# Kernel tuning notes

Measured on AMD Instinct MI355X. Metric: run time of the kernel, lower is better.

Reference implementation:

```python
import jax, jax.numpy as jnp
import numpy as np

STRIDES = (4, 8, 16, 32)
OUT = 7
RATIO = 2  # sampling_ratio per bin dim (ROIAlignV2)
P = OUT * RATIO  # sample points per spatial dim


def _bilinear_axis(coord, size):
    # ROIAlign semantics: zero contribution outside [-1, size], clamp into [0, size-1]
    valid = ((coord > -1.0) & (coord < size)).astype(coord.dtype)
    c = jnp.clip(coord, 0.0, size - 1)
    i0 = jnp.floor(c).astype(jnp.int32)
    i1 = jnp.minimum(i0 + 1, size - 1)
    frac = c - i0.astype(coord.dtype)
    return i0, i1, (1.0 - frac) * valid, frac * valid


def _roi_align(fmap, bidx, boxes, stride):
    """ROIAlignV2 (aligned=True, sampling_ratio=2). fmap: [B,H,W,C], boxes: [N,4] in image coords."""
    H, W = fmap.shape[1], fmap.shape[2]
    x1 = boxes[:, 0] / stride - 0.5
    y1 = boxes[:, 1] / stride - 0.5
    x2 = boxes[:, 2] / stride - 0.5
    y2 = boxes[:, 3] / stride - 0.5
    steps = (jnp.arange(P, dtype=fmap.dtype) + 0.5) / P  # [P] uniform sample centers
    px = x1[:, None] + (x2 - x1)[:, None] * steps  # [N,P]
    py = y1[:, None] + (y2 - y1)[:, None] * steps  # [N,P]
    ix0, ix1, wx0, wx1 = _bilinear_axis(px, W)
    iy0, iy1, wy0, wy1 = _bilinear_axis(py, H)
    b = bidx[:, None, None]

    def g(yi, xi):
        return fmap[b, yi[:, :, None], xi[:, None, :]]  # [N,P,P,C]

    val = ((wy0[:, :, None] * wx0[:, None, :])[..., None] * g(iy0, ix0)
           + (wy0[:, :, None] * wx1[:, None, :])[..., None] * g(iy0, ix1)
           + (wy1[:, :, None] * wx0[:, None, :])[..., None] * g(iy1, ix0)
           + (wy1[:, :, None] * wx1[:, None, :])[..., None] * g(iy1, ix1))
    N, C = boxes.shape[0], fmap.shape[3]
    pooled = val.reshape(N, OUT, RATIO, OUT, RATIO, C).mean(axis=(2, 4))  # avg within each bin
    return pooled.transpose(0, 3, 1, 2).reshape(N, C * OUT * OUT)  # torch [N,C,7,7].flatten(1)


def _head(fms, rois, fc1_w, fc1_b, fc2_w, fc2_b, p_w, p_b):
    bidx = rois[:, 0].astype(jnp.int32)
    boxes = rois[:, 1:5]
    w = boxes[:, 2] - boxes[:, 0]
    h = boxes[:, 3] - boxes[:, 1]
    # standard FPN level assignment: k = floor(4 + log2(sqrt(area)/224)), clamp [2,5]
    k = jnp.floor(4.0 + jnp.log2(jnp.sqrt(jnp.maximum(w * h, 1e-6)) / 224.0))
    lvl = jnp.clip(k, 2.0, 5.0).astype(jnp.int32) - 2  # 0->stride4 ... 3->stride32
    pooled = jnp.stack([_roi_align(fm.transpose(0, 2, 3, 1), bidx, boxes, s)
                        for fm, s in zip(fms, STRIDES)])  # [4,N,D]
    pool5 = pooled[lvl, jnp.arange(rois.shape[0])]  # [N,D] select per-roi level
    fc1 = jax.nn.relu(pool5 @ fc1_w.T + fc1_b)
    fc2 = jax.nn.relu(fc1 @ fc2_w.T + fc2_b)
    return fc2 @ p_w.T + p_b  # prob: [N, 5*n*nheads]


def setup_inputs():
    key = jax.random.key(0)
    ks = jax.random.split(key, 12)
    B, C = 2, 256
    ImH, ImW = 768, 1280
    N = 1024
    NUM_CLASSES, NHEADS = 2, 2
    D = C * OUT * OUT
    fms = [jax.random.normal(ks[i], (B, C, ImH // s, ImW // s), dtype=jnp.float32)
           for i, s in enumerate(STRIDES)]
    # boxes with log-uniform sizes in [32, 512] px, clipped to image
    wh = jnp.exp(jax.random.uniform(ks[4], (N, 2), minval=float(np.log(32.0)), maxval=float(np.log(512.0))))
    cxy = jax.random.uniform(ks[5], (N, 2)) * jnp.array([ImW, ImH], jnp.float32)
    x1 = jnp.clip(cxy[:, 0] - wh[:, 0] / 2, 0.0, ImW - 2.0)
    y1 = jnp.clip(cxy[:, 1] - wh[:, 1] / 2, 0.0, ImH - 2.0)
    x2 = jnp.clip(cxy[:, 0] + wh[:, 0] / 2, x1 + 1.0, ImW - 1.0)
    y2 = jnp.clip(cxy[:, 1] + wh[:, 1] / 2, y1 + 1.0, ImH - 1.0)
    bidx = jax.random.randint(ks[6], (N,), 0, B).astype(jnp.float32)
    rois = jnp.stack([bidx, x1, y1, x2, y2], axis=1)
    fc1_w = jax.random.normal(ks[7], (1024, D), dtype=jnp.float32) / np.sqrt(D).astype(np.float32)
    fc1_b = jnp.zeros((1024,), jnp.float32)
    fc2_w = jax.random.normal(ks[8], (1024, 1024), dtype=jnp.float32) / 32.0
    fc2_b = jnp.zeros((1024,), jnp.float32)
    p_w = jax.random.normal(ks[9], (5 * NUM_CLASSES * NHEADS, 1024), dtype=jnp.float32) / 32.0
    p_b = jnp.zeros((5 * NUM_CLASSES * NHEADS,), jnp.float32)
    return {"fm0": fms[0], "fm1": fms[1], "fm2": fms[2], "fm3": fms[3], "rois": rois,
            "fc1_w": fc1_w, "fc1_b": fc1_b, "fc2_w": fc2_w, "fc2_b": fc2_b,
            "p_w": p_w, "p_b": p_b}


def reference(fm0, fm1, fm2, fm3, rois, fc1_w, fc1_b, fc2_w, fc2_b, p_w, p_b):
    return _head((fm0, fm1, fm2, fm3), rois, fc1_w, fc1_b, fc2_w, fc2_b, p_w, p_b)
```

## Files before the change

### kernel.cpp

```cpp
#include <hip/hip_runtime.h>
#include <hip/hip_bf16.h>
#include <cstddef>
#include <cstdint>


#define NROIS 1024
#define C_CH  256
#define OUTP  7
#define DFEAT (C_CH * OUTP * OUTP)
#define HID   1024
#define NCLS  20

__device__ __forceinline__ unsigned short f2bf(float x) {
    union { float f; uint32_t u; } v; v.f = x;
    uint32_t r = v.u + 0x7fffu + ((v.u >> 16) & 1u);
    return (unsigned short)(r >> 16);
}
__device__ __forceinline__ float bf2f(unsigned short h) {
    union { uint32_t u; float f; } v; v.u = ((uint32_t)h) << 16;
    return v.f;
}

__device__ __forceinline__ void g2lds16(const void* g, void* l) {
    __builtin_amdgcn_global_load_lds(
        (const __attribute__((address_space(1))) void*)g,
        (__attribute__((address_space(3))) void*)l,
        16, 0, 0);
}

typedef __attribute__((ext_vector_type(8))) short bf16x8;
typedef __attribute__((ext_vector_type(4))) float f32x4;

__global__ __launch_bounds__(256) void roi_pool_split(
    const float* __restrict__ fm0, const float* __restrict__ fm1,
    const float* __restrict__ fm2, const float* __restrict__ fm3,
    const float* __restrict__ rois,
    unsigned short* __restrict__ ph, unsigned short* __restrict__ pl)
{
    const int roi = blockIdx.x;
    const int cq  = blockIdx.y;
    const int t   = threadIdx.x;

    __shared__ float s_box[5];
    __shared__ int   s_ix0[16], s_ix1[16], s_iy0[16], s_iy1[16];
    __shared__ float s_wx0[16], s_wx1[16], s_wy0[16], s_wy1[16];

    if (t < 5) s_box[t] = rois[(size_t)roi * 5 + t];
    __syncthreads();

    const int   b   = (int)s_box[0];
    const float bx1 = s_box[1], by1 = s_box[2], bx2 = s_box[3], by2 = s_box[4];

    const float w = bx2 - bx1, h = by2 - by1;
    float kf = floorf(4.0f + log2f(sqrtf(fmaxf(w * h, 1e-6f)) / 224.0f));
    kf = fminf(fmaxf(kf, 2.0f), 5.0f);
    const int lvl    = (int)kf - 2;
    const int stride = 4 << lvl;
    const int H  = 768  / stride;
    const int Wd = 1280 / stride;
    const float* fm = (lvl == 0) ? fm0 : (lvl == 1) ? fm1 : (lvl == 2) ? fm2 : fm3;

    if (t < 14) {
        const float x1s = bx1 / (float)stride - 0.5f;
        const float x2s = bx2 / (float)stride - 0.5f;
        const float coord = x1s + (x2s - x1s) * (((float)t + 0.5f) / 14.0f);
        const float valid = (coord > -1.0f && coord < (float)Wd) ? 1.0f : 0.0f;
        const float cc = fminf(fmaxf(coord, 0.0f), (float)(Wd - 1));
        const int i0 = (int)floorf(cc);
        s_ix0[t] = i0; s_ix1[t] = min(i0 + 1, Wd - 1);
        const float fr = cc - (float)i0;
        s_wx0[t] = (1.0f - fr) * valid; s_wx1[t] = fr * valid;
    } else if (t >= 16 && t < 30) {
        const int j = t - 16;
        const float y1s = by1 / (float)stride - 0.5f;
        const float y2s = by2 / (float)stride - 0.5f;
        const float coord = y1s + (y2s - y1s) * (((float)j + 0.5f) / 14.0f);
        const float valid = (coord > -1.0f && coord < (float)H) ? 1.0f : 0.0f;
        const float cc = fminf(fmaxf(coord, 0.0f), (float)(H - 1));
        const int i0 = (int)floorf(cc);
        s_iy0[j] = i0; s_iy1[j] = min(i0 + 1, H - 1);
        const float fr = cc - (float)i0;
        s_wy0[j] = (1.0f - fr) * valid; s_wy1[j] = fr * valid;
    }
    __syncthreads();

    const int wv = t >> 6, lane = t & 63;
    const int jx = lane & 15, grp = lane >> 4;
    const int xj = min(jx, 13);
    const int x0 = s_ix0[xj], x1 = s_ix1[xj];
    const float wx0 = s_wx0[xj], wx1 = s_wx1[xj];
    const bool xact = (jx < 14);
    const bool wlane = ((grp & 1) == 0) && ((jx & 1) == 0) && xact;

    int   y0r[4], y1r[4];
    float a0r[4], a1r[4];
    bool  yact[4];
    #pragma unroll
    for (int ky = 0; ky < 4; ++ky) {
        const int jy = ky * 4 + grp;
        const int yj = min(jy, 13);
        y0r[ky] = s_iy0[yj]; y1r[ky] = s_iy1[yj];
        a0r[ky] = s_wy0[yj]; a1r[ky] = s_wy1[yj];
        yact[ky] = (jy < 14);
    }

    const size_t hw = (size_t)H * Wd;
    const float* fmb = fm + (size_t)b * C_CH * hw;
    const int c0 = cq * 64 + wv * 16;

    #pragma unroll 2
    for (int ci = 0; ci < 16; ++ci) {
        const int c = c0 + ci;
        const float* fb = fmb + (size_t)c * hw;
        #pragma unroll
        for (int ky = 0; ky < 4; ++ky) {
            const float* r0 = fb + (size_t)y0r[ky] * Wd;
            const float* r1 = fb + (size_t)y1r[ky] * Wd;
            float v = a0r[ky] * (wx0 * r0[x0] + wx1 * r0[x1])
                    + a1r[ky] * (wx0 * r1[x0] + wx1 * r1[x1]);
            if (!xact || !yact[ky]) v = 0.0f;
            v += __shfl_down(v, 1);
            v += __shfl_down(v, 16);
            if (wlane) {
                const int by = ky * 2 + (grp >> 1);
                if (by < 7) {
                    const int bx = jx >> 1;
                    const float r = v * 0.25f;
                    const size_t d = (size_t)roi * DFEAT + c * 49 + by * 7 + bx;
                    const unsigned short hh = f2bf(r);
                    ph[d] = hh;
                    pl[d] = f2bf(r - bf2f(hh));
                }
            }
        }
    }
}

__global__ __launch_bounds__(256) void split_fp32_bf16(
    const float* __restrict__ w, unsigned short* __restrict__ h,
    unsigned short* __restrict__ l, int n4)
{
    int i = blockIdx.x * 256 + threadIdx.x;
    const int stride = gridDim.x * 256;
    for (; i < n4; i += stride) {
        const float4 v = *(const float4*)(w + (size_t)i * 4);
        ushort4 hh, ll;
        hh.x = f2bf(v.x); ll.x = f2bf(v.x - bf2f(hh.x));
        hh.y = f2bf(v.y); ll.y = f2bf(v.y - bf2f(hh.y));
        hh.z = f2bf(v.z); ll.z = f2bf(v.z - bf2f(hh.z));
        hh.w = f2bf(v.w); ll.w = f2bf(v.w - bf2f(hh.w));
        *(ushort4*)(h + (size_t)i * 4) = hh;
        *(ushort4*)(l + (size_t)i * 4) = ll;
    }
}

#define GBM 128
#define GBN 128
#define GBK 32

__global__ __launch_bounds__(256) void gemm_bf16x3(
    const unsigned short* __restrict__ Ah, const unsigned short* __restrict__ Al,
    const unsigned short* __restrict__ Bh, const unsigned short* __restrict__ Bl,
    float* __restrict__ part, int K, int ksplit)
{
    __shared__ __align__(16) unsigned short sAh[GBM * GBK];
    __shared__ __align__(16) unsigned short sAl[GBM * GBK];
    __shared__ __align__(16) unsigned short sBh[GBN * GBK];
    __shared__ __align__(16) unsigned short sBl[GBN * GBK];

    const int t  = threadIdx.x;
    const int bm = blockIdx.y * GBM, bn = blockIdx.x * GBN;
    const int k0 = blockIdx.z * ksplit, k1 = k0 + ksplit;
    const int lane = t & 63, wv = t >> 6;
    const int wr = wv >> 1, wc = wv & 1;
    const int lm = lane & 15, quad = lane >> 4;

    f32x4 acc[4][4] = {};

    const int srow = t >> 2;
    const int skc  = (t & 3) * 8;

    for (int kk = k0; kk < k1; kk += GBK) {
        #pragma unroll
        for (int q = 0; q < 2; ++q) {
            const int row = q * 64 + srow;
            const size_t ga = (size_t)(bm + row) * K + kk + skc;
            const size_t gb = (size_t)(bn + row) * K + kk + skc;
            const int lo = q * 4096 + t * 16;
            g2lds16(Ah + ga, (char*)sAh + lo);
            g2lds16(Al + ga, (char*)sAl + lo);
            g2lds16(Bh + gb, (char*)sBh + lo);
            g2lds16(Bl + gb, (char*)sBl + lo);
        }
        __syncthreads();

        bf16x8 fah[4], fal[4], fbh[4], fbl[4];
        #pragma unroll
        for (int i = 0; i < 4; ++i) {
            fah[i] = *(const bf16x8*)&sAh[(wr * 64 + i * 16 + lm) * GBK + quad * 8];
            fal[i] = *(const bf16x8*)&sAl[(wr * 64 + i * 16 + lm) * GBK + quad * 8];
            fbh[i] = *(const bf16x8*)&sBh[(wc * 64 + i * 16 + lm) * GBK + quad * 8];
            fbl[i] = *(const bf16x8*)&sBl[(wc * 64 + i * 16 + lm) * GBK + quad * 8];
        }
        #pragma unroll
        for (int i = 0; i < 4; ++i)
            #pragma unroll
            for (int j = 0; j < 4; ++j)
                acc[i][j] = __builtin_amdgcn_mfma_f32_16x16x32_bf16(fah[i], fbh[j], acc[i][j], 0, 0, 0);
        #pragma unroll
        for (int i = 0; i < 4; ++i)
            #pragma unroll
            for (int j = 0; j < 4; ++j)
                acc[i][j] = __builtin_amdgcn_mfma_f32_16x16x32_bf16(fah[i], fbl[j], acc[i][j], 0, 0, 0);
        #pragma unroll
        for (int i = 0; i < 4; ++i)
            #pragma unroll
            for (int j = 0; j < 4; ++j)
                acc[i][j] = __builtin_amdgcn_mfma_f32_16x16x32_bf16(fal[i], fbh[j], acc[i][j], 0, 0, 0);
        __syncthreads();
    }

    float* out = part + (size_t)blockIdx.z * (HID * NROIS);
    #pragma unroll
    for (int i = 0; i < 4; ++i) {
        const int mbase = bm + wr * 64 + i * 16 + quad * 4;
        #pragma unroll
        for (int j = 0; j < 4; ++j) {
            const int n = bn + wc * 64 + j * 16 + lm;
            #pragma unroll
            for (int r = 0; r < 4; ++r)
                out[(size_t)(mbase + r) * HID + n] = acc[i][j][r];
        }
    }
}

__global__ __launch_bounds__(256) void reduce_bias_relu(
    const float* __restrict__ part, const float* __restrict__ bias,
    int S, int mode, unsigned short* __restrict__ oh,
    unsigned short* __restrict__ ol, float* __restrict__ ofp)
{
    const int i4 = blockIdx.x * 256 + threadIdx.x;
    const size_t off = (size_t)i4 * 4;
    const int n = (int)(off & (HID - 1));
    float4 s = *(const float4*)(part + off);
    for (int z = 1; z < S; ++z) {
        const float4 p = *(const float4*)(part + (size_t)z * HID * NROIS + off);
        s.x += p.x; s.y += p.y; s.z += p.z; s.w += p.w;
    }
    const float4 b = *(const float4*)(bias + n);
    s.x = fmaxf(s.x + b.x, 0.0f);
    s.y = fmaxf(s.y + b.y, 0.0f);
    s.z = fmaxf(s.z + b.z, 0.0f);
    s.w = fmaxf(s.w + b.w, 0.0f);
    if (mode == 0) {
        *(float4*)(ofp + off) = s;
    } else {
        ushort4 hh, ll;
        hh.x = f2bf(s.x); ll.x = f2bf(s.x - bf2f(hh.x));
        hh.y = f2bf(s.y); ll.y = f2bf(s.y - bf2f(hh.y));
        hh.z = f2bf(s.z); ll.z = f2bf(s.z - bf2f(hh.z));
        hh.w = f2bf(s.w); ll.w = f2bf(s.w - bf2f(hh.w));
        *(ushort4*)(oh + off) = hh;
        *(ushort4*)(ol + off) = ll;
    }
}

__global__ __launch_bounds__(256) void pred_kernel(
    const float* __restrict__ A, const float* __restrict__ Wm,
    const float* __restrict__ bias, float* __restrict__ out)
{
    const int i = blockIdx.x;
    const int t = threadIdx.x;
    const int j = t & 31;
    const int s = t >> 5;

    __shared__ float red[8][32];

    float acc = 0.0f;
    if (j < NCLS) {
        const float4* a4 = (const float4*)(A  + (size_t)i * HID + s * 128);
        const float4* w4 = (const float4*)(Wm + (size_t)j * HID + s * 128);
        #pragma unroll 8
        for (int q = 0; q < 32; ++q) {
            const float4 a = a4[q], w = w4[q];
            acc += a.x * w.x + a.y * w.y + a.z * w.z + a.w * w.w;
        }
    }
    red[s][j] = acc;
    __syncthreads();
    if (s == 0 && j < NCLS) {
        float v = bias[j];
        #pragma unroll
        for (int q = 0; q < 8; ++q) v += red[q][j];
        out[(size_t)i * NCLS + j] = v;
    }
}

extern "C" void kernel_launch(void* const* d_in, const int* in_sizes, int n_in,
                              void* d_out, int out_size, void* d_ws, size_t ws_size,
                              hipStream_t stream) {
    (void)in_sizes; (void)n_in; (void)out_size;

    const float* fm0   = (const float*)d_in[0];
    const float* fm1   = (const float*)d_in[1];
    const float* fm2   = (const float*)d_in[2];
    const float* fm3   = (const float*)d_in[3];
    const float* rois  = (const float*)d_in[4];
    const float* fc1_w = (const float*)d_in[5];
    const float* fc1_b = (const float*)d_in[6];
    const float* fc2_w = (const float*)d_in[7];
    const float* fc2_b = (const float*)d_in[8];
    const float* p_w   = (const float*)d_in[9];
    const float* p_b   = (const float*)d_in[10];

    const size_t SZ_POOL = (size_t)NROIS * DFEAT * 2;
    const size_t SZ_W1   = (size_t)HID * DFEAT * 2;
    const size_t SZ_W2   = (size_t)HID * HID * 2;
    const size_t SZ_FC1  = (size_t)NROIS * HID * 2;
    const size_t SZ_FC2O = (size_t)NROIS * HID * 4;
    const size_t SZ_PART1 = (size_t)HID * NROIS * 4;

    const size_t fixed = 2 * SZ_POOL + 2 * SZ_W1 + 2 * SZ_W2 + 2 * SZ_FC1 + SZ_FC2O;
    int S1 = 8;
    while (S1 > 1 && fixed + (size_t)S1 * SZ_PART1 > ws_size) S1 >>= 1;
    const int S2 = (S1 < 4) ? S1 : 4;

    char* p = (char*)d_ws;
    unsigned short* ph   = (unsigned short*)p; p += SZ_POOL;
    unsigned short* pl   = (unsigned short*)p; p += SZ_POOL;
    unsigned short* w1h  = (unsigned short*)p; p += SZ_W1;
    unsigned short* w1l  = (unsigned short*)p; p += SZ_W1;
    unsigned short* w2h  = (unsigned short*)p; p += SZ_W2;
    unsigned short* w2l  = (unsigned short*)p; p += SZ_W2;
    unsigned short* fc1h = (unsigned short*)p; p += SZ_FC1;
    unsigned short* fc1l = (unsigned short*)p; p += SZ_FC1;
    float* fc2o = (float*)p; p += SZ_FC2O;
    float* part = (float*)p;

    float* outp = (float*)d_out;

    split_fp32_bf16<<<4096, 256, 0, stream>>>(fc1_w, w1h, w1l, HID * DFEAT / 4);
    split_fp32_bf16<<<1024, 256, 0, stream>>>(fc2_w, w2h, w2l, HID * HID / 4);

    roi_pool_split<<<dim3(NROIS, 4), 256, 0, stream>>>(fm0, fm1, fm2, fm3, rois, ph, pl);

    {
        dim3 grid(HID / GBN, NROIS / GBM, S1);
        gemm_bf16x3<<<grid, 256, 0, stream>>>(ph, pl, w1h, w1l, part, DFEAT, DFEAT / S1);
    }
    reduce_bias_relu<<<NROIS * HID / 4 / 256, 256, 0, stream>>>(
        part, fc1_b, S1, 1, fc1h, fc1l, (float*)nullptr);

    {
        dim3 grid(HID / GBN, NROIS / GBM, S2);
        gemm_bf16x3<<<grid, 256, 0, stream>>>(fc1h, fc1l, w2h, w2l, part, HID, HID / S2);
    }
    reduce_bias_relu<<<NROIS * HID / 4 / 256, 256, 0, stream>>>(
        part, fc2_b, S2, 0, (unsigned short*)nullptr, (unsigned short*)nullptr, fc2o);

    pred_kernel<<<NROIS, 256, 0, stream>>>(fc2o, p_w, p_b, outp);
}
```

Before: 554.4 us.

## Transpose feature maps to NHWC and permute fc1 weights for coalesced ROI pooling

```diff
diff --git a/kernel.cpp b/kernel.cpp
--- a/kernel.cpp
+++ b/kernel.cpp
@@ -11,6 +11,12 @@
 #define HID   1024
 #define NCLS  20
 
+#define NHWC_OFF0 0
+#define NHWC_OFF1 31457280
+#define NHWC_OFF2 39321600
+#define NHWC_OFF3 41287680
+#define NHWC_TOT  41779200
+
 __device__ __forceinline__ unsigned short f2bf(float x) {
     union { float f; uint32_t u; } v; v.f = x;
     uint32_t r = v.u + 0x7fffu + ((v.u >> 16) & 1u);
@@ -31,14 +37,51 @@
 typedef __attribute__((ext_vector_type(8))) short bf16x8;
 typedef __attribute__((ext_vector_type(4))) float f32x4;
 
-__global__ __launch_bounds__(256) void roi_pool_split(
-    const float* __restrict__ fm0, const float* __restrict__ fm1,
-    const float* __restrict__ fm2, const float* __restrict__ fm3,
-    const float* __restrict__ rois,
+__global__ __launch_bounds__(256) void nchw_to_nhwc(
+    const float* __restrict__ in, float* __restrict__ out, int H, int W)
+{
+    __shared__ float s[64][69];
+
+    const int t  = threadIdx.x;
+    const int x0 = blockIdx.x * 64;
+    const int y  = blockIdx.y;
+    const int ct = blockIdx.z & 3;
+    const int b  = blockIdx.z >> 2;
+    const int c0 = ct * 64;
+
+    const int tx = t & 15, ty = t >> 4;
+
+    #pragma unroll
+    for (int q = 0; q < 4; ++q) {
+        const int row = ty + q * 16;
+        const int x = x0 + tx * 4;
+        if (x < W) {
+            const float4 v = *(const float4*)(in +
+                (((size_t)(b * C_CH + c0 + row) * H + y) * W + x));
+            s[row][tx * 4 + 0] = v.x; s[row][tx * 4 + 1] = v.y;
+            s[row][tx * 4 + 2] = v.z; s[row][tx * 4 + 3] = v.w;
+        }
+    }
+    __syncthreads();
+
+    #pragma unroll
+    for (int q = 0; q < 4; ++q) {
+        const int j = ty + q * 16;
+        const int x = x0 + j;
+        if (x < W) {
+            float4 v;
+            v.x = s[tx * 4 + 0][j]; v.y = s[tx * 4 + 1][j];
+            v.z = s[tx * 4 + 2][j]; v.w = s[tx * 4 + 3][j];
+            *(float4*)(out + (((size_t)(b * H + y) * W + x) * C_CH + c0 + tx * 4)) = v;
+        }
+    }
+}
+
+__global__ __launch_bounds__(256) void roi_pool_nhwc(
+    const float* __restrict__ nh, const float* __restrict__ rois,
     unsigned short* __restrict__ ph, unsigned short* __restrict__ pl)
 {
     const int roi = blockIdx.x;
-    const int cq  = blockIdx.y;
     const int t   = threadIdx.x;
 
     __shared__ float s_box[5];
@@ -58,7 +101,10 @@
     const int stride = 4 << lvl;
     const int H  = 768  / stride;
     const int Wd = 1280 / stride;
-    const float* fm = (lvl == 0) ? fm0 : (lvl == 1) ? fm1 : (lvl == 2) ? fm2 : fm3;
+
+    const size_t lvloff = (lvl == 0) ? NHWC_OFF0 : (lvl == 1) ? NHWC_OFF1
+                        : (lvl == 2) ? NHWC_OFF2 : NHWC_OFF3;
+    const float* base = nh + lvloff + (size_t)b * H * Wd * C_CH;
 
     if (t < 14) {
         const float x1s = bx1 / (float)stride - 0.5f;
@@ -85,6 +131,99 @@
     __syncthreads();
 
     const int wv = t >> 6, lane = t & 63;
+    const int g  = blockIdx.y * 4 + wv;
+    const int c4 = lane * 4;
+
+    for (int bin = g; bin < 49; bin += 8) {
+        const int by = bin / 7, bx = bin - by * 7;
+        float ax = 0.0f, ay = 0.0f, az = 0.0f, aw = 0.0f;
+        #pragma unroll
+        for (int sy = 0; sy < 2; ++sy) {
+            const int jy = by * 2 + sy;
+            const int y0 = s_iy0[jy], y1 = s_iy1[jy];
+            const float a0 = s_wy0[jy], a1 = s_wy1[jy];
+            #pragma unroll
+            for (int sx = 0; sx < 2; ++sx) {
+                const int jx = bx * 2 + sx;
+                const int x0 = s_ix0[jx], x1 = s_ix1[jx];
+                const float b0 = s_wx0[jx], b1 = s_wx1[jx];
+                const float4 p00 = *(const float4*)(base + ((size_t)(y0 * Wd + x0)) * C_CH + c4);
+                const float4 p01 = *(const float4*)(base + ((size_t)(y0 * Wd + x1)) * C_CH + c4);
+                const float4 p10 = *(const float4*)(base + ((size_t)(y1 * Wd + x0)) * C_CH + c4);
+                const float4 p11 = *(const float4*)(base + ((size_t)(y1 * Wd + x1)) * C_CH + c4);
+                const float w00 = a0 * b0, w01 = a0 * b1, w10 = a1 * b0, w11 = a1 * b1;
+                ax += w00 * p00.x + w01 * p01.x + w10 * p10.x + w11 * p11.x;
+                ay += w00 * p00.y + w01 * p01.y + w10 * p10.y + w11 * p11.y;
+                az += w00 * p00.z + w01 * p01.z + w10 * p10.z + w11 * p11.z;
+                aw += w00 * p00.w + w01 * p01.w + w10 * p10.w + w11 * p11.w;
+            }
+        }
+        const float r0 = ax * 0.25f, r1 = ay * 0.25f, r2 = az * 0.25f, r3 = aw * 0.25f;
+        ushort4 hh, ll;
+        hh.x = f2bf(r0); ll.x = f2bf(r0 - bf2f(hh.x));
+        hh.y = f2bf(r1); ll.y = f2bf(r1 - bf2f(hh.y));
+        hh.z = f2bf(r2); ll.z = f2bf(r2 - bf2f(hh.z));
+        hh.w = f2bf(r3); ll.w = f2bf(r3 - bf2f(hh.w));
+        const size_t d = (size_t)roi * DFEAT + (size_t)bin * C_CH + c4;
+        *(ushort4*)(ph + d) = hh;
+        *(ushort4*)(pl + d) = ll;
+    }
+}
+
+__global__ __launch_bounds__(256) void roi_pool_gather(
+    const float* __restrict__ fm0, const float* __restrict__ fm1,
+    const float* __restrict__ fm2, const float* __restrict__ fm3,
+    const float* __restrict__ rois,
+    unsigned short* __restrict__ ph, unsigned short* __restrict__ pl)
+{
+    const int roi = blockIdx.x;
+    const int cq  = blockIdx.y;
+    const int t   = threadIdx.x;
+
+    __shared__ float s_box[5];
+    __shared__ int   s_ix0[16], s_ix1[16], s_iy0[16], s_iy1[16];
+    __shared__ float s_wx0[16], s_wx1[16], s_wy0[16], s_wy1[16];
+
+    if (t < 5) s_box[t] = rois[(size_t)roi * 5 + t];
+    __syncthreads();
+
+    const int   b   = (int)s_box[0];
+    const float bx1 = s_box[1], by1 = s_box[2], bx2 = s_box[3], by2 = s_box[4];
+
+    const float w = bx2 - bx1, h = by2 - by1;
+    float kf = floorf(4.0f + log2f(sqrtf(fmaxf(w * h, 1e-6f)) / 224.0f));
+    kf = fminf(fmaxf(kf, 2.0f), 5.0f);
+    const int lvl    = (int)kf - 2;
+    const int stride = 4 << lvl;
+    const int H  = 768  / stride;
+    const int Wd = 1280 / stride;
+    const float* fm = (lvl == 0) ? fm0 : (lvl == 1) ? fm1 : (lvl == 2) ? fm2 : fm3;
+
+    if (t < 14) {
+        const float x1s = bx1 / (float)stride - 0.5f;
+        const float x2s = bx2 / (float)stride - 0.5f;
+        const float coord = x1s + (x2s - x1s) * (((float)t + 0.5f) / 14.0f);
+        const float valid = (coord > -1.0f && coord < (float)Wd) ? 1.0f : 0.0f;
+        const float cc = fminf(fmaxf(coord, 0.0f), (float)(Wd - 1));
+        const int i0 = (int)floorf(cc);
+        s_ix0[t] = i0; s_ix1[t] = min(i0 + 1, Wd - 1);
+        const float fr = cc - (float)i0;
+        s_wx0[t] = (1.0f - fr) * valid; s_wx1[t] = fr * valid;
+    } else if (t >= 16 && t < 30) {
+        const int j = t - 16;
+        const float y1s = by1 / (float)stride - 0.5f;
+        const float y2s = by2 / (float)stride - 0.5f;
+        const float coord = y1s + (y2s - y1s) * (((float)j + 0.5f) / 14.0f);
+        const float valid = (coord > -1.0f && coord < (float)H) ? 1.0f : 0.0f;
+        const float cc = fminf(fmaxf(coord, 0.0f), (float)(H - 1));
+        const int i0 = (int)floorf(cc);
+        s_iy0[j] = i0; s_iy1[j] = min(i0 + 1, H - 1);
+        const float fr = cc - (float)i0;
+        s_wy0[j] = (1.0f - fr) * valid; s_wy1[j] = fr * valid;
+    }
+    __syncthreads();
+
+    const int wv = t >> 6, lane = t & 63;
     const int jx = lane & 15, grp = lane >> 4;
     const int xj = min(jx, 13);
     const int x0 = s_ix0[xj], x1 = s_ix1[xj];
@@ -126,13 +265,42 @@
                 if (by < 7) {
                     const int bx = jx >> 1;
                     const float r = v * 0.25f;
-                    const size_t d = (size_t)roi * DFEAT + c * 49 + by * 7 + bx;
+                    const size_t d = (size_t)roi * DFEAT + (size_t)(by * 7 + bx) * C_CH + c;
                     const unsigned short hh = f2bf(r);
                     ph[d] = hh;
                     pl[d] = f2bf(r - bf2f(hh));
                 }
             }
         }
+    }
+}
+
+__global__ __launch_bounds__(256) void split_permute_w1(
+    const float* __restrict__ w, unsigned short* __restrict__ oh,
+    unsigned short* __restrict__ ol)
+{
+    __shared__ unsigned short sh[3136], sl[3136];
+
+    const int t  = threadIdx.x;
+    const int ct = blockIdx.x;
+    const int n  = blockIdx.y;
+
+    const float* src = w + (size_t)n * DFEAT + (size_t)ct * 64 * 49;
+    for (int e4 = t; e4 < 784; e4 += 256) {
+        const float4 v = *(const float4*)(src + e4 * 4);
+        unsigned short hx = f2bf(v.x), hy = f2bf(v.y), hz = f2bf(v.z), hw = f2bf(v.w);
+        sh[e4 * 4 + 0] = hx; sl[e4 * 4 + 0] = f2bf(v.x - bf2f(hx));
+        sh[e4 * 4 + 1] = hy; sl[e4 * 4 + 1] = f2bf(v.y - bf2f(hy));
+        sh[e4 * 4 + 2] = hz; sl[e4 * 4 + 2] = f2bf(v.z - bf2f(hz));
+        sh[e4 * 4 + 3] = hw; sl[e4 * 4 + 3] = f2bf(v.w - bf2f(hw));
+    }
+    __syncthreads();
+
+    for (int e = t; e < 3136; e += 256) {
+        const int bin = e >> 6, c = e & 63;
+        const size_t d = (size_t)n * DFEAT + (size_t)bin * C_CH + ct * 64 + c;
+        oh[d] = sh[c * 49 + bin];
+        ol[d] = sl[c * 49 + bin];
     }
 }
 
@@ -313,16 +481,20 @@
     const float* p_w   = (const float*)d_in[9];
     const float* p_b   = (const float*)d_in[10];
 
-    const size_t SZ_POOL = (size_t)NROIS * DFEAT * 2;
-    const size_t SZ_W1   = (size_t)HID * DFEAT * 2;
-    const size_t SZ_W2   = (size_t)HID * HID * 2;
-    const size_t SZ_FC1  = (size_t)NROIS * HID * 2;
-    const size_t SZ_FC2O = (size_t)NROIS * HID * 4;
+    const size_t SZ_POOL  = (size_t)NROIS * DFEAT * 2;
+    const size_t SZ_W1    = (size_t)HID * DFEAT * 2;
+    const size_t SZ_W2    = (size_t)HID * HID * 2;
+    const size_t SZ_FC1   = (size_t)NROIS * HID * 2;
+    const size_t SZ_FC2O  = (size_t)NROIS * HID * 4;
     const size_t SZ_PART1 = (size_t)HID * NROIS * 4;
+    const size_t SZ_NHWC  = (size_t)NHWC_TOT * 4;
 
     const size_t fixed = 2 * SZ_POOL + 2 * SZ_W1 + 2 * SZ_W2 + 2 * SZ_FC1 + SZ_FC2O;
+
+    const int use_nhwc = (ws_size >= fixed + SZ_NHWC + SZ_PART1) ? 1 : 0;
+    const size_t avail_part = ws_size - fixed - (use_nhwc ? SZ_NHWC : 0);
     int S1 = 8;
-    while (S1 > 1 && fixed + (size_t)S1 * SZ_PART1 > ws_size) S1 >>= 1;
+    while (S1 > 1 && (size_t)S1 * SZ_PART1 > avail_part) S1 >>= 1;
     const int S2 = (S1 < 4) ? S1 : 4;
 
     char* p = (char*)d_ws;
@@ -335,14 +507,23 @@
     unsigned short* fc1h = (unsigned short*)p; p += SZ_FC1;
     unsigned short* fc1l = (unsigned short*)p; p += SZ_FC1;
     float* fc2o = (float*)p; p += SZ_FC2O;
-    float* part = (float*)p;
+    float* part = (float*)p; p += (size_t)S1 * SZ_PART1;
+    float* nhwc = (float*)p;
 
     float* outp = (float*)d_out;
 
-    split_fp32_bf16<<<4096, 256, 0, stream>>>(fc1_w, w1h, w1l, HID * DFEAT / 4);
+    split_permute_w1<<<dim3(4, 1024), 256, 0, stream>>>(fc1_w, w1h, w1l);
     split_fp32_bf16<<<1024, 256, 0, stream>>>(fc2_w, w2h, w2l, HID * HID / 4);
 
-    roi_pool_split<<<dim3(NROIS, 4), 256, 0, stream>>>(fm0, fm1, fm2, fm3, rois, ph, pl);
+    if (use_nhwc) {
+        nchw_to_nhwc<<<dim3(5, 192, 8), 256, 0, stream>>>(fm0, nhwc + NHWC_OFF0, 192, 320);
+        nchw_to_nhwc<<<dim3(3,  96, 8), 256, 0, stream>>>(fm1, nhwc + NHWC_OFF1,  96, 160);
+        nchw_to_nhwc<<<dim3(2,  48, 8), 256, 0, stream>>>(fm2, nhwc + NHWC_OFF2,  48,  80);
+        nchw_to_nhwc<<<dim3(1,  24, 8), 256, 0, stream>>>(fm3, nhwc + NHWC_OFF3,  24,  40);
+        roi_pool_nhwc<<<dim3(NROIS, 2), 256, 0, stream>>>(nhwc, rois, ph, pl);
+    } else {
+        roi_pool_gather<<<dim3(NROIS, 4), 256, 0, stream>>>(fm0, fm1, fm2, fm3, rois, ph, pl);
+    }
 
     {
         dim3 grid(HID / GBN, NROIS / GBM, S1);
```

After: 540.8 us. 1.03x faster.
